# Performance work log

Hardware: AMD Instinct MI355X
Metric: run time of the kernel (lower is better)

The kernel has to match this reference:

```python
import jax, jax.numpy as jnp
import numpy as np

B, T, E = 8, 2048, 1024
H = 16
HD = E // H            # per-head hidden_dim = 64
DFF = 4 * E
DC = T // 512          # decay_constant = 4
EPS = 1e-5


def setup_inputs() -> dict:
    key = jax.random.key(0)
    ks = jax.random.split(key, 8)
    return {
        "x": jax.random.normal(ks[0], (B, T, E), jnp.float32),
        # per-head input projections (Linear(dim, hidden_dim) x H)
        "w_proj": jax.random.normal(ks[1], (H, E, HD), jnp.float32) / np.sqrt(E),
        "b_proj": jnp.zeros((H, HD), jnp.float32),
        # causal mixing weights: first H//2 heads are Col-repeat, last H//2 Row-repeat
        "mix_w": jax.random.normal(ks[2], (H, T), jnp.float32),
        "mix_b": jnp.zeros((H, T), jnp.float32),
        "decay": jnp.ones((H,), jnp.float32),   # decay_value params (init ones as in torch)
        "out_w": jax.random.normal(ks[3], (E, E), jnp.float32) / np.sqrt(E),
        "out_b": jnp.zeros((E,), jnp.float32),
        "ln1_g": jnp.ones((E,), jnp.float32),
        "ln1_b": jnp.zeros((E,), jnp.float32),
        "ln2_g": jnp.ones((E,), jnp.float32),
        "ln2_b": jnp.zeros((E,), jnp.float32),
        "ff_w1": jax.random.normal(ks[4], (E, DFF), jnp.float32) / np.sqrt(E),
        "ff_b1": jnp.zeros((DFF,), jnp.float32),
        "ff_w2": jax.random.normal(ks[5], (DFF, E), jnp.float32) / np.sqrt(DFF),
        "ff_b2": jnp.zeros((E,), jnp.float32),
        "index": 0,
    }


def _layernorm(x, g, b):
    mu = jnp.mean(x, -1, keepdims=True)
    var = jnp.var(x, -1, keepdims=True)
    return (x - mu) * jax.lax.rsqrt(var + EPS) * g + b


def _mix_matrices(mix_w, decay):
    # Col heads: M[i,j] = v[j] * d**((j-i)/DC) for j>=i else 0
    # Row heads: M[i,j] = v[i] * d**((j-i)/DC) for j>=i else 0
    i = jnp.arange(T)[:, None]
    j = jnp.arange(T)[None, :]
    d = jnp.clip(decay, 0.9, 1.0)                                   # (H,)
    expo = (j - i).astype(jnp.float32) / DC                         # (T,T)
    dec = d[:, None, None] ** expo                                  # (H,T,T)
    causal = (j >= i)
    half = H // 2
    Mcol = jnp.where(causal, mix_w[:half, None, :] * dec[:half], 0.0)
    Mrow = jnp.where(causal, mix_w[half:, :, None] * dec[half:], 0.0)
    return jnp.concatenate([Mcol, Mrow], axis=0)                    # (H,T,T)


def reference(x, w_proj, b_proj, mix_w, mix_b, decay, out_w, out_b,
              ln1_g, ln1_b, ln2_g, ln2_b, ff_w1, ff_b1, ff_w2, ff_b2, index):
    # ---- token-mixing sub-block (parallel path of MixedRepeatHeads) ----
    res = x
    h = _layernorm(x, ln1_g, ln1_b)
    # per-head projection: (B,T,E) x (H,E,HD) -> (B,H,T,HD)
    p = jnp.einsum('bte,hef->bhtf', h, w_proj) + b_proj[:, None, :]
    M = _mix_matrices(mix_w, decay)
    # causal decay mixing along time: out[b,h,s,f] = sum_t p[b,h,t,f] * M[h,t,s]
    mixed = jnp.einsum('bhtf,hts->bhsf', p, M) + mix_b[None, :, :, None]
    # concat heads along feature dim -> (B,T,E)
    mixed = mixed.transpose(0, 2, 1, 3).reshape(B, T, E)
    mixed = mixed @ out_w + out_b
    x = mixed + res
    # ---- feed-forward sub-block ----
    res = x
    h = _layernorm(x, ln2_g, ln2_b)
    h = jax.nn.gelu(h @ ff_w1 + ff_b1) @ ff_w2 + ff_b2
    return h + res
```

## Files before the change

### kernel.cpp

```cpp
#include <hip/hip_runtime.h>


#define TT 2048
#define EE 1024
#define HHD 64
#define MROWS 16384
#define SC_L 64

typedef __bf16 bf16x8 __attribute__((ext_vector_type(8)));
typedef float f32x4 __attribute__((ext_vector_type(4)));
typedef unsigned short u16;
typedef unsigned int u32;

__device__ __forceinline__ u16 f2bf(float f) {
  u32 u = __builtin_bit_cast(u32, f);
  u += 0x7FFFu + ((u >> 16) & 1u);
  return (u16)(u >> 16);
}
__device__ __forceinline__ float bf2f(u16 s) {
  u32 u = ((u32)s) << 16;
  return __builtin_bit_cast(float, u);
}
__device__ __forceinline__ float gelu_f(float x) {
  float x2 = x * x;
  float e = -1.5957691216057308f * x * __builtin_fmaf(0.044715f, x2, 1.0f);
  return x * __builtin_amdgcn_rcpf(1.0f + __expf(e));
}
__device__ __forceinline__ void gload_lds16(const void* g, void* l) {
  __builtin_amdgcn_global_load_lds(
      (const __attribute__((address_space(1))) u32*)g,
      (__attribute__((address_space(3))) u32*)l, 16, 0, 0);
}
__device__ __forceinline__ void wg_barrier() {
  asm volatile("" ::: "memory");
  __builtin_amdgcn_s_barrier();
  asm volatile("" ::: "memory");
}

__global__ __launch_bounds__(256) void transpose_to_bf16(
    const float* __restrict__ src, u16* __restrict__ dst, int R, int C,
    long sbs, long dbs) {
  __shared__ float tile[32][33];
  src += (long)blockIdx.z * sbs;
  dst += (long)blockIdx.z * dbs;
  int c0 = blockIdx.x * 32, r0 = blockIdx.y * 32;
  int tx = threadIdx.x, ty = threadIdx.y;
#pragma unroll
  for (int i = 0; i < 4; i++)
    tile[ty + i * 8][tx] = src[(long)(r0 + ty + i * 8) * C + c0 + tx];
  __syncthreads();
#pragma unroll
  for (int i = 0; i < 4; i++)
    dst[(long)(c0 + ty + i * 8) * R + r0 + tx] = f2bf(tile[tx][ty + i * 8]);
}

__global__ __launch_bounds__(256) void ln_to_bf16(
    const float* __restrict__ x, const float* __restrict__ gam,
    const float* __restrict__ bet, u16* __restrict__ y) {
  int row = blockIdx.x;
  int tid = threadIdx.x;
  float4 v = ((const float4*)x)[row * 256 + tid];
  float s = v.x + v.y + v.z + v.w;
  float s2 = v.x * v.x + v.y * v.y + v.z * v.z + v.w * v.w;
#pragma unroll
  for (int off = 1; off < 64; off <<= 1) {
    s += __shfl_xor(s, off);
    s2 += __shfl_xor(s2, off);
  }
  __shared__ float red[8];
  int w = tid >> 6;
  if ((tid & 63) == 0) { red[w] = s; red[4 + w] = s2; }
  __syncthreads();
  s = red[0] + red[1] + red[2] + red[3];
  s2 = red[4] + red[5] + red[6] + red[7];
  float mu = s * (1.0f / 1024.0f);
  float var = s2 * (1.0f / 1024.0f) - mu * mu;
  float rstd = rsqrtf(var + 1e-5f);
  int e0 = tid * 4;
  ushort4 o;
  o.x = f2bf((v.x - mu) * rstd * gam[e0 + 0] + bet[e0 + 0]);
  o.y = f2bf((v.y - mu) * rstd * gam[e0 + 1] + bet[e0 + 1]);
  o.z = f2bf((v.z - mu) * rstd * gam[e0 + 2] + bet[e0 + 2]);
  o.w = f2bf((v.w - mu) * rstd * gam[e0 + 3] + bet[e0 + 3]);
  ((ushort4*)y)[row * 256 + tid] = o;
}

template <int EPI>
__global__ __launch_bounds__(512, 2) void gemm256(
    const u16* __restrict__ A, const u16* __restrict__ Bt,
    const float* __restrict__ bias, const float* __restrict__ res, void* outp,
    int M, int N, int K, int px, int gxp, int byper) {
  __shared__ u16 lds[65536];
  const int tid = threadIdx.x;
  const int w = tid >> 6, lane = tid & 63;
  const int wm = w >> 2, wn = w & 3;
  const int l15 = lane & 15, lk = lane >> 4;

  const int gx = (int)gridDim.x;
  const int bid = (int)blockIdx.y * gx + (int)blockIdx.x;
  const int xcd = bid & 7, i = bid >> 3;
  const int xg = xcd % gxp, yg = xcd / gxp;
  const int bx = xg * px + (i % px);
  const int by = yg * byper + (i / px);
  const int m0 = by * 256, n0 = bx * 256;

  const int srow = w * 8 + (lane >> 3);
  const int sslot = (lane & 7) ^ (lane >> 3);
  const u16* aS = A + (size_t)(m0 + srow) * K + sslot * 8;
  const u16* bS = Bt + (size_t)(n0 + srow) * K + sslot * 8;

  f32x4 acc[8][4];
  const f32x4 z = {0.f, 0.f, 0.f, 0.f};
#pragma unroll
  for (int mi = 0; mi < 8; mi++)
#pragma unroll
    for (int ni = 0; ni < 4; ni++) acc[mi][ni] = z;

  bf16x8 a[4], b0[4], b1[4];

#define STAGE_B(C, KT, H) { \
    u16* lb = lds + (C) * 32768 + 16384 + (H) * 8192 + w * 512; \
    gload_lds16(bS + (size_t)((H) * 128) * K + (KT), lb); \
    gload_lds16(bS + (size_t)((H) * 128 + 64) * K + (KT), lb + 4096); }

#define STAGE_A02(C, KT) { \
    u16* lb = lds + (C) * 32768 + w * 512; \
    gload_lds16(aS + (KT), lb); \
    gload_lds16(aS + (size_t)128 * K + (KT), lb + 8192); }

#define STAGE_A13(C, KT) { \
    u16* lb = lds + (C) * 32768 + 4096 + w * 512; \
    gload_lds16(aS + (size_t)64 * K + (KT), lb); \
    gload_lds16(aS + (size_t)192 * K + (KT), lb + 8192); }

#define RD_A(C, KS, MH) { \
    const bf16x8* lp = (const bf16x8*)(lds + (C) * 32768); \
    const int sl = ((KS) * 4 + lk) ^ (l15 & 7); \
    const int rb = wm * 128 + (MH) * 64 + l15; \
    a[0] = lp[rb * 8 + sl]; \
    a[1] = lp[(rb + 16) * 8 + sl]; \
    a[2] = lp[(rb + 32) * 8 + sl]; \
    a[3] = lp[(rb + 48) * 8 + sl]; }

#define RD_B(BV, C, KS) { \
    const bf16x8* lp = (const bf16x8*)(lds + (C) * 32768 + 16384); \
    const int sl = ((KS) * 4 + lk) ^ (l15 & 7); \
    const int rb = wn * 64 + l15; \
    BV[0] = lp[rb * 8 + sl]; \
    BV[1] = lp[(rb + 16) * 8 + sl]; \
    BV[2] = lp[(rb + 32) * 8 + sl]; \
    BV[3] = lp[(rb + 48) * 8 + sl]; }

#define MFMA16(MH, BV) { \
    __builtin_amdgcn_s_setprio(1); \
    _Pragma("unroll") \
    for (int mm = 0; mm < 4; mm++) \
      _Pragma("unroll") \
      for (int nn = 0; nn < 4; nn++) \
        acc[(MH) * 4 + mm][nn] = __builtin_amdgcn_mfma_f32_16x16x32_bf16( \
            a[mm], BV[nn], acc[(MH) * 4 + mm][nn], 0, 0, 0); \
    __builtin_amdgcn_s_setprio(0); }

  const int nt = K >> 6;
  STAGE_B(0, 0, 0);
  STAGE_B(0, 0, 1);
  STAGE_A02(0, 0);
  STAGE_A13(0, 0);
  asm volatile("s_waitcnt vmcnt(0)" ::: "memory");
  wg_barrier();

  int cur = 0;
  for (int t = 0; t < nt - 1; ++t) {
    const int kn = (t + 1) << 6;
    const int nx = cur ^ 1;
    RD_B(b0, cur, 0);
    RD_A(cur, 0, 0);
    STAGE_B(nx, kn, 0);
    STAGE_B(nx, kn, 1);
    STAGE_A02(nx, kn);
    wg_barrier();
    MFMA16(0, b0);
    wg_barrier();
    RD_B(b1, cur, 1);
    RD_A(cur, 1, 0);
    STAGE_A13(nx, kn);
    wg_barrier();
    MFMA16(0, b1);
    asm volatile("s_waitcnt vmcnt(8)" ::: "memory");
    wg_barrier();
    RD_A(cur, 0, 1);
    wg_barrier();
    MFMA16(1, b0);
    wg_barrier();
    RD_A(cur, 1, 1);
    wg_barrier();
    MFMA16(1, b1);
    asm volatile("s_waitcnt vmcnt(2)" ::: "memory");
    wg_barrier();
    cur = nx;
  }
  RD_B(b0, cur, 0);
  RD_A(cur, 0, 0);
  MFMA16(0, b0);
  RD_B(b1, cur, 1);
  RD_A(cur, 1, 0);
  MFMA16(0, b1);
  asm volatile("s_waitcnt vmcnt(0)" ::: "memory");
  wg_barrier();
  RD_A(cur, 0, 1);
  MFMA16(1, b0);
  RD_A(cur, 1, 1);
  MFMA16(1, b1);
#undef STAGE_B
#undef STAGE_A02
#undef STAGE_A13
#undef RD_A
#undef RD_B
#undef MFMA16

#pragma unroll
  for (int mi = 0; mi < 8; mi++) {
#pragma unroll
    for (int ni = 0; ni < 4; ni++) {
      int n = n0 + wn * 64 + ni * 16 + l15;
      float bvv = bias[n];
#pragma unroll
      for (int r = 0; r < 4; r++) {
        int m = m0 + wm * 128 + mi * 16 + lk * 4 + r;
        size_t idx = (size_t)m * N + n;
        float v = acc[mi][ni][r] + bvv;
        if (EPI == 0) {
          ((u16*)outp)[idx] = f2bf(v);
        } else if (EPI == 1) {
          ((float*)outp)[idx] = v + res[idx];
        } else {
          ((u16*)outp)[idx] = f2bf(gelu_f(v));
        }
      }
    }
  }
}

__global__ __launch_bounds__(64) void scan_carry(
    const u16* __restrict__ p, const float* __restrict__ mix_w,
    const float* __restrict__ decay, float* __restrict__ carry) {
  int blk = blockIdx.x;
  int c = blk & 31, h = (blk >> 5) & 15, b = blk >> 9;
  int f = threadIdx.x;
  float d = fminf(fmaxf(decay[h], 0.9f), 1.0f);
  float r = powf(d, 0.25f);
  size_t base = ((size_t)b * TT + c * SC_L) * EE + h * HHD + f;
  const float* mw = mix_w + h * TT + c * SC_L;
  bool isRow = (h >= 8);
  float S = 0.f;
#pragma unroll 4
  for (int t = 0; t < SC_L; t++) {
    float pv = bf2f(p[base + (size_t)t * EE]);
    float q = isRow ? mw[t] * pv : pv;
    S = r * S + q;
  }
  carry[blk * 64 + f] = S;
}

__global__ __launch_bounds__(64) void scan_apply(
    const u16* __restrict__ p, const float* __restrict__ mix_w,
    const float* __restrict__ mix_b, const float* __restrict__ decay,
    const float* __restrict__ carry, u16* __restrict__ mixed) {
  int blk = blockIdx.x;
  int c = blk & 31, h = (blk >> 5) & 15, b = blk >> 9;
  int f = threadIdx.x;
  float d = fminf(fmaxf(decay[h], 0.9f), 1.0f);
  float r = powf(d, 0.25f);
  float rl = powf(r, (float)SC_L);
  int cb = blk - c;
  float S = 0.f;
  for (int cc = 0; cc < c; cc++) S = rl * S + carry[(cb + cc) * 64 + f];
  size_t base = ((size_t)b * TT + c * SC_L) * EE + h * HHD + f;
  const float* mw = mix_w + h * TT + c * SC_L;
  const float* mb = mix_b + h * TT + c * SC_L;
  bool isRow = (h >= 8);
  for (int t = 0; t < SC_L; t++) {
    float pv = bf2f(p[base + (size_t)t * EE]);
    float q = isRow ? mw[t] * pv : pv;
    S = r * S + q;
    float val = (isRow ? S : mw[t] * S) + mb[t];
    mixed[base + (size_t)t * EE] = f2bf(val);
  }
}

extern "C" void kernel_launch(void* const* d_in, const int* in_sizes, int n_in,
                              void* d_out, int out_size, void* d_ws, size_t ws_size,
                              hipStream_t stream) {
  const float* x = (const float*)d_in[0];
  const float* w_proj = (const float*)d_in[1];
  const float* b_proj = (const float*)d_in[2];
  const float* mix_w = (const float*)d_in[3];
  const float* mix_b = (const float*)d_in[4];
  const float* decay = (const float*)d_in[5];
  const float* out_w = (const float*)d_in[6];
  const float* out_b = (const float*)d_in[7];
  const float* ln1_g = (const float*)d_in[8];
  const float* ln1_b = (const float*)d_in[9];
  const float* ln2_g = (const float*)d_in[10];
  const float* ln2_b = (const float*)d_in[11];
  const float* ff_w1 = (const float*)d_in[12];
  const float* ff_b1 = (const float*)d_in[13];
  const float* ff_w2 = (const float*)d_in[14];
  const float* ff_b2 = (const float*)d_in[15];
  float* out = (float*)d_out;

  char* ws = (char*)d_ws;
  const size_t MiB = 1ull << 20;
  u16* wWp = (u16*)(ws + 0 * MiB);
  u16* wWo = (u16*)(ws + 2 * MiB);
  u16* wW1 = (u16*)(ws + 4 * MiB);
  u16* wW2 = (u16*)(ws + 12 * MiB);
  u16* wMix = (u16*)(ws + 20 * MiB);
  u16* wH = (u16*)(ws + 52 * MiB);
  u16* wP = (u16*)(ws + 84 * MiB);
  u16* wU = (u16*)(ws + 52 * MiB);
  float* wCarry = (float*)(ws + 180 * MiB);

  dim3 tb(32, 8);
  transpose_to_bf16<<<dim3(2, 32, 16), tb, 0, stream>>>(w_proj, wWp, 1024, 64,
                                                        65536L, 65536L);
  transpose_to_bf16<<<dim3(32, 32, 1), tb, 0, stream>>>(out_w, wWo, 1024, 1024, 0L, 0L);
  transpose_to_bf16<<<dim3(128, 32, 1), tb, 0, stream>>>(ff_w1, wW1, 1024, 4096, 0L, 0L);
  transpose_to_bf16<<<dim3(32, 128, 1), tb, 0, stream>>>(ff_w2, wW2, 4096, 1024, 0L, 0L);

  ln_to_bf16<<<dim3(MROWS), dim3(256), 0, stream>>>(x, ln1_g, ln1_b, wH);

  gemm256<0><<<dim3(4, 64), dim3(512), 0, stream>>>(
      wH, wWp, b_proj, (const float*)nullptr, (void*)wP, MROWS, 1024, 1024,
      4, 1, 8);

  scan_carry<<<dim3(4096), dim3(64), 0, stream>>>(wP, mix_w, decay, wCarry);
  scan_apply<<<dim3(4096), dim3(64), 0, stream>>>(wP, mix_w, mix_b, decay, wCarry, wMix);

  gemm256<1><<<dim3(4, 64), dim3(512), 0, stream>>>(
      wMix, wWo, out_b, x, (void*)out, MROWS, 1024, 1024,
      4, 1, 8);

  ln_to_bf16<<<dim3(MROWS), dim3(256), 0, stream>>>(out, ln2_g, ln2_b, wMix);

  gemm256<2><<<dim3(16, 64), dim3(512), 0, stream>>>(
      wMix, wW1, ff_b1, (const float*)nullptr, (void*)wU, MROWS, 4096, 1024,
      4, 4, 32);

  gemm256<1><<<dim3(4, 64), dim3(512), 0, stream>>>(
      wU, wW2, ff_b2, out, (void*)out, MROWS, 1024, 4096,
      2, 2, 16);
}
```

Before: 530.8 us.

## Restructure GEMM main loop into four M-quarter phases with interleaved prefetch

New measurement: 542.9 us. 1.02x slower.

```diff
diff --git a/kernel.cpp b/kernel.cpp
--- a/kernel.cpp
+++ b/kernel.cpp
@@ -116,7 +116,11 @@
 #pragma unroll
     for (int ni = 0; ni < 4; ni++) acc[mi][ni] = z;
 
-  bf16x8 a[4], b0[4], b1[4];
+  bf16x8 a[4];
+  bf16x8 bq[2][4];
+
+  const int sl0 = (lk ^ (l15 & 7)) * 8;
+  const int sl1 = ((4 + lk) ^ (l15 & 7)) * 8;
 
 #define STAGE_B(C, KT, H) { \
     u16* lb = lds + (C) * 32768 + 16384 + (H) * 8192 + w * 512; \
@@ -133,32 +137,35 @@
     gload_lds16(aS + (size_t)64 * K + (KT), lb); \
     gload_lds16(aS + (size_t)192 * K + (KT), lb + 8192); }
 
-#define RD_A(C, KS, MH) { \
-    const bf16x8* lp = (const bf16x8*)(lds + (C) * 32768); \
-    const int sl = ((KS) * 4 + lk) ^ (l15 & 7); \
-    const int rb = wm * 128 + (MH) * 64 + l15; \
-    a[0] = lp[rb * 8 + sl]; \
-    a[1] = lp[(rb + 16) * 8 + sl]; \
-    a[2] = lp[(rb + 32) * 8 + sl]; \
-    a[3] = lp[(rb + 48) * 8 + sl]; }
-
-#define RD_B(BV, C, KS) { \
-    const bf16x8* lp = (const bf16x8*)(lds + (C) * 32768 + 16384); \
-    const int sl = ((KS) * 4 + lk) ^ (l15 & 7); \
-    const int rb = wn * 64 + l15; \
-    BV[0] = lp[rb * 8 + sl]; \
-    BV[1] = lp[(rb + 16) * 8 + sl]; \
-    BV[2] = lp[(rb + 32) * 8 + sl]; \
-    BV[3] = lp[(rb + 48) * 8 + sl]; }
-
-#define MFMA16(MH, BV) { \
+#define RD_AQ(C, Q) { \
+    const u16* base = lds + (C) * 32768 + (wm * 128 + (Q) * 32 + l15) * 64; \
+    a[0] = *(const bf16x8*)(base + sl0); \
+    a[1] = *(const bf16x8*)(base + sl1); \
+    a[2] = *(const bf16x8*)(base + 16 * 64 + sl0); \
+    a[3] = *(const bf16x8*)(base + 16 * 64 + sl1); }
+
+#define RD_BALL(C) { \
+    const u16* base = lds + (C) * 32768 + 16384 + (wn * 64 + l15) * 64; \
+    _Pragma("unroll") \
+    for (int ni = 0; ni < 4; ni++) { \
+      bq[0][ni] = *(const bf16x8*)(base + ni * 16 * 64 + sl0); \
+      bq[1][ni] = *(const bf16x8*)(base + ni * 16 * 64 + sl1); } }
+
+#define BAR_MID() { \
+    wg_barrier(); \
+    asm volatile("s_waitcnt lgkmcnt(0)" ::: "memory"); \
+    __builtin_amdgcn_sched_barrier(0); }
+
+#define MFMAQ(Q) { \
     __builtin_amdgcn_s_setprio(1); \
     _Pragma("unroll") \
-    for (int mm = 0; mm < 4; mm++) \
+    for (int ks = 0; ks < 2; ks++) \
       _Pragma("unroll") \
-      for (int nn = 0; nn < 4; nn++) \
-        acc[(MH) * 4 + mm][nn] = __builtin_amdgcn_mfma_f32_16x16x32_bf16( \
-            a[mm], BV[nn], acc[(MH) * 4 + mm][nn], 0, 0, 0); \
+      for (int mm = 0; mm < 2; mm++) \
+        _Pragma("unroll") \
+        for (int nn = 0; nn < 4; nn++) \
+          acc[(Q) * 2 + mm][nn] = __builtin_amdgcn_mfma_f32_16x16x32_bf16( \
+              a[mm * 2 + ks], bq[ks][nn], acc[(Q) * 2 + mm][nn], 0, 0, 0); \
     __builtin_amdgcn_s_setprio(0); }
 
   const int nt = K >> 6;
@@ -166,57 +173,50 @@
   STAGE_B(0, 0, 1);
   STAGE_A02(0, 0);
   STAGE_A13(0, 0);
-  asm volatile("s_waitcnt vmcnt(0)" ::: "memory");
+  asm volatile("s_waitcnt vmcnt(2)" ::: "memory");
   wg_barrier();
 
   int cur = 0;
-  for (int t = 0; t < nt - 1; ++t) {
+  for (int t = 0; t < nt; ++t) {
+    const int nx = cur ^ 1;
     const int kn = (t + 1) << 6;
-    const int nx = cur ^ 1;
-    RD_B(b0, cur, 0);
-    RD_A(cur, 0, 0);
-    STAGE_B(nx, kn, 0);
-    STAGE_B(nx, kn, 1);
-    STAGE_A02(nx, kn);
+    const bool pf = (t + 1 < nt);
+    RD_BALL(cur);
+    RD_AQ(cur, 0);
+    if (pf) STAGE_B(nx, kn, 0);
+    BAR_MID();
+    MFMAQ(0);
     wg_barrier();
-    MFMA16(0, b0);
+    RD_AQ(cur, 1);
+    if (pf) STAGE_B(nx, kn, 1);
+    BAR_MID();
+    MFMAQ(1);
+    if (pf) {
+      asm volatile("s_waitcnt vmcnt(4)" ::: "memory");
+    } else {
+      asm volatile("s_waitcnt vmcnt(0)" ::: "memory");
+    }
     wg_barrier();
-    RD_B(b1, cur, 1);
-    RD_A(cur, 1, 0);
-    STAGE_A13(nx, kn);
+    RD_AQ(cur, 2);
+    if (pf) STAGE_A02(nx, kn);
+    BAR_MID();
+    MFMAQ(2);
     wg_barrier();
-    MFMA16(0, b1);
-    asm volatile("s_waitcnt vmcnt(8)" ::: "memory");
-    wg_barrier();
-    RD_A(cur, 0, 1);
-    wg_barrier();
-    MFMA16(1, b0);
-    wg_barrier();
-    RD_A(cur, 1, 1);
-    wg_barrier();
-    MFMA16(1, b1);
+    RD_AQ(cur, 3);
+    if (pf) STAGE_A13(nx, kn);
+    BAR_MID();
+    MFMAQ(3);
     asm volatile("s_waitcnt vmcnt(2)" ::: "memory");
     wg_barrier();
     cur = nx;
   }
-  RD_B(b0, cur, 0);
-  RD_A(cur, 0, 0);
-  MFMA16(0, b0);
-  RD_B(b1, cur, 1);
-  RD_A(cur, 1, 0);
-  MFMA16(0, b1);
-  asm volatile("s_waitcnt vmcnt(0)" ::: "memory");
-  wg_barrier();
-  RD_A(cur, 0, 1);
-  MFMA16(1, b0);
-  RD_A(cur, 1, 1);
-  MFMA16(1, b1);
 #undef STAGE_B
 #undef STAGE_A02
 #undef STAGE_A13
-#undef RD_A
-#undef RD_B
-#undef MFMA16
+#undef RD_AQ
+#undef RD_BALL
+#undef BAR_MID
+#undef MFMAQ
 
 #pragma unroll
   for (int mi = 0; mi < 8; mi++) {
```

## Switch GEMMs to 32x32x16 MFMA and vectorize scan kernels across features

Applied to the files above, without the earlier changes.

New measurement: 550.9 us. 1.04x slower.

```diff
diff --git a/kernel.cpp b/kernel.cpp
--- a/kernel.cpp
+++ b/kernel.cpp
@@ -9,8 +9,10 @@
 
 typedef __bf16 bf16x8 __attribute__((ext_vector_type(8)));
 typedef float f32x4 __attribute__((ext_vector_type(4)));
+typedef float f32x16 __attribute__((ext_vector_type(16)));
 typedef unsigned short u16;
 typedef unsigned int u32;
+typedef u16 u16x8 __attribute__((ext_vector_type(8)));
 
 __device__ __forceinline__ u16 f2bf(float f) {
   u32 u = __builtin_bit_cast(u32, f);
@@ -86,7 +88,7 @@
 }
 
 template <int EPI>
-__global__ __launch_bounds__(512, 2) void gemm256(
+__global__ __launch_bounds__(512, 1) void gemm256m32(
     const u16* __restrict__ A, const u16* __restrict__ Bt,
     const float* __restrict__ bias, const float* __restrict__ res, void* outp,
     int M, int N, int K, int px, int gxp, int byper) {
@@ -94,14 +96,14 @@
   const int tid = threadIdx.x;
   const int w = tid >> 6, lane = tid & 63;
   const int wm = w >> 2, wn = w & 3;
-  const int l15 = lane & 15, lk = lane >> 4;
+  const int l31 = lane & 31, kg = lane >> 5;
+  const int swz = l31 & 7;
 
   const int gx = (int)gridDim.x;
   const int bid = (int)blockIdx.y * gx + (int)blockIdx.x;
   const int xcd = bid & 7, i = bid >> 3;
-  const int xg = xcd % gxp, yg = xcd / gxp;
-  const int bx = xg * px + (i % px);
-  const int by = yg * byper + (i / px);
+  const int bx = (xcd % gxp) * px + (i % px);
+  const int by = (xcd / gxp) * byper + (i / px);
   const int m0 = by * 256, n0 = bx * 256;
 
   const int srow = w * 8 + (lane >> 3);
@@ -109,59 +111,54 @@
   const u16* aS = A + (size_t)(m0 + srow) * K + sslot * 8;
   const u16* bS = Bt + (size_t)(n0 + srow) * K + sslot * 8;
 
-  f32x4 acc[8][4];
-  const f32x4 z = {0.f, 0.f, 0.f, 0.f};
-#pragma unroll
-  for (int mi = 0; mi < 8; mi++)
-#pragma unroll
-    for (int ni = 0; ni < 4; ni++) acc[mi][ni] = z;
-
-  bf16x8 a[4], b0[4], b1[4];
+  f32x16 acc[4][2];
+#pragma unroll
+  for (int mt = 0; mt < 4; mt++)
+#pragma unroll
+    for (int nt = 0; nt < 2; nt++) acc[mt][nt] = (f32x16)(0.f);
+
+  bf16x8 a[2][2], b0[2][2], b1[2][2];
 
 #define STAGE_B(C, KT, H) { \
     u16* lb = lds + (C) * 32768 + 16384 + (H) * 8192 + w * 512; \
     gload_lds16(bS + (size_t)((H) * 128) * K + (KT), lb); \
     gload_lds16(bS + (size_t)((H) * 128 + 64) * K + (KT), lb + 4096); }
-
 #define STAGE_A02(C, KT) { \
     u16* lb = lds + (C) * 32768 + w * 512; \
     gload_lds16(aS + (KT), lb); \
     gload_lds16(aS + (size_t)128 * K + (KT), lb + 8192); }
-
 #define STAGE_A13(C, KT) { \
     u16* lb = lds + (C) * 32768 + 4096 + w * 512; \
     gload_lds16(aS + (size_t)64 * K + (KT), lb); \
     gload_lds16(aS + (size_t)192 * K + (KT), lb + 8192); }
 
-#define RD_A(C, KS, MH) { \
-    const bf16x8* lp = (const bf16x8*)(lds + (C) * 32768); \
-    const int sl = ((KS) * 4 + lk) ^ (l15 & 7); \
-    const int rb = wm * 128 + (MH) * 64 + l15; \
-    a[0] = lp[rb * 8 + sl]; \
-    a[1] = lp[(rb + 16) * 8 + sl]; \
-    a[2] = lp[(rb + 32) * 8 + sl]; \
-    a[3] = lp[(rb + 48) * 8 + sl]; }
-
-#define RD_B(BV, C, KS) { \
-    const bf16x8* lp = (const bf16x8*)(lds + (C) * 32768 + 16384); \
-    const int sl = ((KS) * 4 + lk) ^ (l15 & 7); \
-    const int rb = wn * 64 + l15; \
-    BV[0] = lp[rb * 8 + sl]; \
-    BV[1] = lp[(rb + 16) * 8 + sl]; \
-    BV[2] = lp[(rb + 32) * 8 + sl]; \
-    BV[3] = lp[(rb + 48) * 8 + sl]; }
-
-#define MFMA16(MH, BV) { \
+#define RD_A(C, KH, MH) { \
+    const u16* lp = lds + (C) * 32768; \
+    const int ra = (wm * 128 + (MH) * 64 + l31) * 64; \
+    a[0][0] = *(const bf16x8*)(lp + ra + ((((KH)*4) + kg) ^ swz) * 8); \
+    a[0][1] = *(const bf16x8*)(lp + ra + ((((KH)*4) + 2 + kg) ^ swz) * 8); \
+    a[1][0] = *(const bf16x8*)(lp + ra + 2048 + ((((KH)*4) + kg) ^ swz) * 8); \
+    a[1][1] = *(const bf16x8*)(lp + ra + 2048 + ((((KH)*4) + 2 + kg) ^ swz) * 8); }
+#define RD_B(BV, C, KH) { \
+    const u16* lp = lds + (C) * 32768 + 16384; \
+    const int rb = (wn * 64 + l31) * 64; \
+    BV[0][0] = *(const bf16x8*)(lp + rb + ((((KH)*4) + kg) ^ swz) * 8); \
+    BV[0][1] = *(const bf16x8*)(lp + rb + ((((KH)*4) + 2 + kg) ^ swz) * 8); \
+    BV[1][0] = *(const bf16x8*)(lp + rb + 2048 + ((((KH)*4) + kg) ^ swz) * 8); \
+    BV[1][1] = *(const bf16x8*)(lp + rb + 2048 + ((((KH)*4) + 2 + kg) ^ swz) * 8); }
+#define MFMA8(MH, BV) { \
     __builtin_amdgcn_s_setprio(1); \
     _Pragma("unroll") \
-    for (int mm = 0; mm < 4; mm++) \
+    for (int ks2 = 0; ks2 < 2; ks2++) \
       _Pragma("unroll") \
-      for (int nn = 0; nn < 4; nn++) \
-        acc[(MH) * 4 + mm][nn] = __builtin_amdgcn_mfma_f32_16x16x32_bf16( \
-            a[mm], BV[nn], acc[(MH) * 4 + mm][nn], 0, 0, 0); \
+      for (int mt2 = 0; mt2 < 2; mt2++) \
+        _Pragma("unroll") \
+        for (int nt = 0; nt < 2; nt++) \
+          acc[(MH) * 2 + mt2][nt] = __builtin_amdgcn_mfma_f32_32x32x16_bf16( \
+              a[mt2][ks2], BV[nt][ks2], acc[(MH) * 2 + mt2][nt], 0, 0, 0); \
     __builtin_amdgcn_s_setprio(0); }
 
-  const int nt = K >> 6;
+  const int nt_ = K >> 6;
   STAGE_B(0, 0, 0);
   STAGE_B(0, 0, 1);
   STAGE_A02(0, 0);
@@ -170,7 +167,7 @@
   wg_barrier();
 
   int cur = 0;
-  for (int t = 0; t < nt - 1; ++t) {
+  for (int t = 0; t < nt_ - 1; ++t) {
     const int kn = (t + 1) << 6;
     const int nx = cur ^ 1;
     RD_B(b0, cur, 0);
@@ -179,56 +176,56 @@
     STAGE_B(nx, kn, 1);
     STAGE_A02(nx, kn);
     wg_barrier();
-    MFMA16(0, b0);
+    MFMA8(0, b0);
     wg_barrier();
     RD_B(b1, cur, 1);
     RD_A(cur, 1, 0);
     STAGE_A13(nx, kn);
     wg_barrier();
-    MFMA16(0, b1);
+    MFMA8(0, b1);
     asm volatile("s_waitcnt vmcnt(8)" ::: "memory");
     wg_barrier();
     RD_A(cur, 0, 1);
     wg_barrier();
-    MFMA16(1, b0);
+    MFMA8(1, b0);
     wg_barrier();
     RD_A(cur, 1, 1);
     wg_barrier();
-    MFMA16(1, b1);
+    MFMA8(1, b1);
     asm volatile("s_waitcnt vmcnt(2)" ::: "memory");
     wg_barrier();
     cur = nx;
   }
   RD_B(b0, cur, 0);
   RD_A(cur, 0, 0);
-  MFMA16(0, b0);
+  MFMA8(0, b0);
   RD_B(b1, cur, 1);
   RD_A(cur, 1, 0);
-  MFMA16(0, b1);
+  MFMA8(0, b1);
   asm volatile("s_waitcnt vmcnt(0)" ::: "memory");
   wg_barrier();
   RD_A(cur, 0, 1);
-  MFMA16(1, b0);
+  MFMA8(1, b0);
   RD_A(cur, 1, 1);
-  MFMA16(1, b1);
+  MFMA8(1, b1);
 #undef STAGE_B
 #undef STAGE_A02
 #undef STAGE_A13
 #undef RD_A
 #undef RD_B
-#undef MFMA16
-
-#pragma unroll
-  for (int mi = 0; mi < 8; mi++) {
-#pragma unroll
-    for (int ni = 0; ni < 4; ni++) {
-      int n = n0 + wn * 64 + ni * 16 + l15;
+#undef MFMA8
+
+#pragma unroll
+  for (int mt = 0; mt < 4; mt++) {
+#pragma unroll
+    for (int nt = 0; nt < 2; nt++) {
+      int n = n0 + wn * 64 + nt * 32 + l31;
       float bvv = bias[n];
 #pragma unroll
-      for (int r = 0; r < 4; r++) {
-        int m = m0 + wm * 128 + mi * 16 + lk * 4 + r;
+      for (int reg = 0; reg < 16; reg++) {
+        int m = m0 + wm * 128 + mt * 32 + (reg & 3) + 8 * (reg >> 2) + 4 * kg;
         size_t idx = (size_t)m * N + n;
-        float v = acc[mi][ni][r] + bvv;
+        float v = acc[mt][nt][reg] + bvv;
         if (EPI == 0) {
           ((u16*)outp)[idx] = f2bf(v);
         } else if (EPI == 1) {
@@ -244,47 +241,62 @@
 __global__ __launch_bounds__(64) void scan_carry(
     const u16* __restrict__ p, const float* __restrict__ mix_w,
     const float* __restrict__ decay, float* __restrict__ carry) {
-  int blk = blockIdx.x;
-  int c = blk & 31, h = (blk >> 5) & 15, b = blk >> 9;
-  int f = threadIdx.x;
+  int chunk = blockIdx.x * 8 + (threadIdx.x >> 3);
+  int fg = threadIdx.x & 7;
+  int c = chunk & 31, h = (chunk >> 5) & 15, b = chunk >> 9;
   float d = fminf(fmaxf(decay[h], 0.9f), 1.0f);
   float r = powf(d, 0.25f);
-  size_t base = ((size_t)b * TT + c * SC_L) * EE + h * HHD + f;
+  size_t base = (((size_t)b * TT + c * SC_L) * EE + h * HHD + fg * 8) >> 3;
+  const u16x8* p8 = (const u16x8*)p;
   const float* mw = mix_w + h * TT + c * SC_L;
   bool isRow = (h >= 8);
-  float S = 0.f;
-#pragma unroll 4
+  float S[8] = {0.f, 0.f, 0.f, 0.f, 0.f, 0.f, 0.f, 0.f};
   for (int t = 0; t < SC_L; t++) {
-    float pv = bf2f(p[base + (size_t)t * EE]);
-    float q = isRow ? mw[t] * pv : pv;
-    S = r * S + q;
-  }
-  carry[blk * 64 + f] = S;
+    u16x8 v = p8[base + (size_t)t * (EE / 8)];
+    float wv = isRow ? mw[t] : 1.0f;
+#pragma unroll
+    for (int j = 0; j < 8; j++) S[j] = r * S[j] + wv * bf2f(v[j]);
+  }
+  float* cp = carry + chunk * 64 + fg * 8;
+#pragma unroll
+  for (int j = 0; j < 8; j++) cp[j] = S[j];
 }
 
 __global__ __launch_bounds__(64) void scan_apply(
     const u16* __restrict__ p, const float* __restrict__ mix_w,
     const float* __restrict__ mix_b, const float* __restrict__ decay,
     const float* __restrict__ carry, u16* __restrict__ mixed) {
-  int blk = blockIdx.x;
-  int c = blk & 31, h = (blk >> 5) & 15, b = blk >> 9;
-  int f = threadIdx.x;
+  int chunk = blockIdx.x * 8 + (threadIdx.x >> 3);
+  int fg = threadIdx.x & 7;
+  int c = chunk & 31, h = (chunk >> 5) & 15, b = chunk >> 9;
   float d = fminf(fmaxf(decay[h], 0.9f), 1.0f);
   float r = powf(d, 0.25f);
   float rl = powf(r, (float)SC_L);
-  int cb = blk - c;
-  float S = 0.f;
-  for (int cc = 0; cc < c; cc++) S = rl * S + carry[(cb + cc) * 64 + f];
-  size_t base = ((size_t)b * TT + c * SC_L) * EE + h * HHD + f;
+  int cb = chunk - c;
+  float S[8] = {0.f, 0.f, 0.f, 0.f, 0.f, 0.f, 0.f, 0.f};
+  for (int cc = 0; cc < c; cc++) {
+    const float* cp = carry + (cb + cc) * 64 + fg * 8;
+#pragma unroll
+    for (int j = 0; j < 8; j++) S[j] = rl * S[j] + cp[j];
+  }
+  size_t base = (((size_t)b * TT + c * SC_L) * EE + h * HHD + fg * 8) >> 3;
+  const u16x8* p8 = (const u16x8*)p;
+  u16x8* m8 = (u16x8*)mixed;
   const float* mw = mix_w + h * TT + c * SC_L;
   const float* mb = mix_b + h * TT + c * SC_L;
   bool isRow = (h >= 8);
   for (int t = 0; t < SC_L; t++) {
-    float pv = bf2f(p[base + (size_t)t * EE]);
-    float q = isRow ? mw[t] * pv : pv;
-    S = r * S + q;
-    float val = (isRow ? S : mw[t] * S) + mb[t];
-    mixed[base + (size_t)t * EE] = f2bf(val);
+    u16x8 v = p8[base + (size_t)t * (EE / 8)];
+    float wq = isRow ? mw[t] : 1.0f;
+    float wo = isRow ? 1.0f : mw[t];
+    float bb = mb[t];
+    u16x8 o;
+#pragma unroll
+    for (int j = 0; j < 8; j++) {
+      S[j] = r * S[j] + wq * bf2f(v[j]);
+      o[j] = f2bf(wo * S[j] + bb);
+    }
+    m8[base + (size_t)t * (EE / 8)] = o;
   }
 }
 
@@ -330,24 +342,24 @@
 
   ln_to_bf16<<<dim3(MROWS), dim3(256), 0, stream>>>(x, ln1_g, ln1_b, wH);
 
-  gemm256<0><<<dim3(4, 64), dim3(512), 0, stream>>>(
+  gemm256m32<0><<<dim3(4, 64), dim3(512), 0, stream>>>(
       wH, wWp, b_proj, (const float*)nullptr, (void*)wP, MROWS, 1024, 1024,
       4, 1, 8);
 
-  scan_carry<<<dim3(4096), dim3(64), 0, stream>>>(wP, mix_w, decay, wCarry);
-  scan_apply<<<dim3(4096), dim3(64), 0, stream>>>(wP, mix_w, mix_b, decay, wCarry, wMix);
-
-  gemm256<1><<<dim3(4, 64), dim3(512), 0, stream>>>(
+  scan_carry<<<dim3(512), dim3(64), 0, stream>>>(wP, mix_w, decay, wCarry);
+  scan_apply<<<dim3(512), dim3(64), 0, stream>>>(wP, mix_w, mix_b, decay, wCarry, wMix);
+
+  gemm256m32<1><<<dim3(4, 64), dim3(512), 0, stream>>>(
       wMix, wWo, out_b, x, (void*)out, MROWS, 1024, 1024,
       4, 1, 8);
 
   ln_to_bf16<<<dim3(MROWS), dim3(256), 0, stream>>>(out, ln2_g, ln2_b, wMix);
 
-  gemm256<2><<<dim3(16, 64), dim3(512), 0, stream>>>(
+  gemm256m32<2><<<dim3(16, 64), dim3(512), 0, stream>>>(
       wMix, wW1, ff_b1, (const float*)nullptr, (void*)wU, MROWS, 4096, 1024,
       4, 4, 32);
 
-  gemm256<1><<<dim3(4, 64), dim3(512), 0, stream>>>(
+  gemm256m32<1><<<dim3(4, 64), dim3(512), 0, stream>>>(
       wU, wW2, ff_b2, out, (void*)out, MROWS, 1024, 4096,
       2, 2, 16);
 }
```
